# Performance work log

Hardware: AMD Instinct MI355X
Metric: run time of the kernel (lower is better)

The kernel has to match this reference:

```python
import jax, jax.numpy as jnp
import numpy as np

PARAM = 10.0
EPS = 1e-06

def _feature_map(t):
    # elus_feature_map: param*relu(x) + (exp(param*min(x,0)) - 1) + 1
    x1 = jax.nn.relu(t)
    x2 = t - x1  # negative part
    return PARAM * x1 + jnp.exp(PARAM * x2)

def setup_inputs() -> dict:
    key = jax.random.key(0)
    ks = jax.random.split(key, 7)
    B, C, H, W = 8, 512, 128, 128
    d = C // 8
    s = 1.0 / np.sqrt(C)
    return {
        "x":  jax.random.normal(ks[0], (B, C, H, W), dtype=jnp.float32),
        "Wq": jax.random.normal(ks[1], (d, C), dtype=jnp.float32) * s,
        "bq": jax.random.normal(ks[2], (d,), dtype=jnp.float32) * 0.01,
        "Wk": jax.random.normal(ks[3], (d, C), dtype=jnp.float32) * s,
        "bk": jax.random.normal(ks[4], (d,), dtype=jnp.float32) * 0.01,
        "Wv": jax.random.normal(ks[5], (C, C), dtype=jnp.float32) * s,
        "bv": jax.random.normal(ks[6], (C,), dtype=jnp.float32) * 0.01,
        "gamma": jnp.full((1,), 0.5, dtype=jnp.float32),
    }

def reference(x, Wq, bq, Wk, bk, Wv, bv, gamma):
    B, C, H, W = x.shape
    N = H * W
    xf = x.reshape(B, C, N)  # flatten spatial; 1x1 convs become matmuls
    Q = jnp.einsum('dc,bcn->bdn', Wq, xf) + bq[None, :, None]   # [B, d, N]
    K = jnp.einsum('dc,bcn->bdn', Wk, xf) + bk[None, :, None]   # [B, d, N]
    V = jnp.einsum('oc,bcn->bon', Wv, xf) + bv[None, :, None]   # [B, C, N]
    Q = jnp.transpose(_feature_map(Q), (0, 2, 1))               # [B, N, d]
    K = _feature_map(K)                                         # [B, d, N]
    KV = jnp.einsum('bmn,bcn->bmc', K, V)                       # [B, d, C]
    norm = 1.0 / jnp.einsum('bnc,bc->bn', Q, jnp.sum(K, axis=-1) + EPS)  # [B, N]
    wv = jnp.einsum('bnm,bmc,bn->bcn', Q, KV, norm)             # [B, C, N]
    wv = wv.reshape(B, C, H, W)
    return x + gamma * wv
```

## Files before the change

kernel.cpp:

```cpp
#include <hip/hip_runtime.h>
#include <hip/hip_bf16.h>
#include <cstdint>

typedef __bf16 bf16x8 __attribute__((ext_vector_type(8)));
typedef float f32x4 __attribute__((ext_vector_type(4)));

#define DEV static __device__ __forceinline__

constexpr int NB = 8;
constexpr int NC = 512;
constexpr int NS = 16384;
constexpr int ND = 64;
constexpr int SK = 32;
constexpr float FPARAM = 10.0f;
constexpr float FEPS = 1e-6f;

DEV unsigned short f2bf(float f) {
  uint32_t u = __builtin_bit_cast(uint32_t, f);
  u += 0x7fffu + ((u >> 16) & 1u);
  return (unsigned short)(u >> 16);
}
DEV float bf2f(unsigned short h) {
  uint32_t u = ((uint32_t)h) << 16;
  return __builtin_bit_cast(float, u);
}
DEV float fmap(float t) {
  float p = fmaxf(t, 0.0f);
  float m = fminf(t, 0.0f);
  return FPARAM * p + __expf(FPARAM * m);
}

DEV void tile_store4(unsigned short* t, int row, int k, ushort4 v) {
  int ch = (k >> 3) ^ (row & 7);
  *(ushort4*)(t + row * 64 + ch * 8 + (k & 7)) = v;
}
DEV void tile_store8(unsigned short* t, int row, int k, uint4 v) {
  int ch = (k >> 3) ^ (row & 7);
  *(uint4*)(t + row * 64 + ch * 8) = v;
}
DEV bf16x8 tile_frag(const unsigned short* t, int row, int k) {
  int ch = (k >> 3) ^ (row & 7);
  uint4 u = *(const uint4*)(t + row * 64 + ch * 8);
  return __builtin_bit_cast(bf16x8, u);
}
DEV f32x4 mfma16(bf16x8 a, bf16x8 b, f32x4 c) {
  return __builtin_amdgcn_mfma_f32_16x16x32_bf16(a, b, c, 0, 0, 0);
}

__global__ __launch_bounds__(256) void kernelA(
    const float* __restrict__ x, const float* __restrict__ Wq,
    const float* __restrict__ bq, const float* __restrict__ Wk,
    const float* __restrict__ bk, unsigned short* __restrict__ Kp,
    unsigned short* __restrict__ Qt) {
  __shared__ unsigned short sW[128 * 64];
  __shared__ unsigned short sX[128 * 64];
  const int t = threadIdx.x;
  const int lane = t & 63, wave = t >> 6;
  const int wm = wave >> 1, wn = wave & 1;
  const int l15 = lane & 15, q = lane >> 4;
  const int n0 = blockIdx.x * 128;
  const int b = blockIdx.y;
  const float* xb = x + (size_t)b * NC * NS;

  f32x4 acc[4][4];
  const f32x4 zero = {0.f, 0.f, 0.f, 0.f};
  for (int i = 0; i < 4; i++)
    for (int j = 0; j < 4; j++) acc[i][j] = zero;

  const int qq = t & 3, grp = t >> 2;
  const int n4 = (grp & 31) * 4, cb = (grp >> 5) * 4;
  const int shfl_base = (t & 63) & ~3;

  for (int c0 = 0; c0 < NC; c0 += 64) {
    __syncthreads();
    {
      int f4 = t & 15;
      for (int it = 0; it < 8; it++) {
        int row = (t >> 4) + it * 16;
        const float* src = (row < 64) ? (Wq + (size_t)row * NC + c0 + f4 * 4)
                                      : (Wk + (size_t)(row - 64) * NC + c0 + f4 * 4);
        float4 v = *(const float4*)src;
        tile_store4(sW, row, f4 * 4,
                    make_ushort4(f2bf(v.x), f2bf(v.y), f2bf(v.z), f2bf(v.w)));
      }
    }
    for (int it = 0; it < 8; it++) {
      int c_l = cb + qq + it * 8;
      float4 v = *(const float4*)(xb + (size_t)(c0 + c_l) * NS + n0 + n4);
      float vv[4] = {v.x, v.y, v.z, v.w};
      float o[4];
      for (int r = 0; r < 4; r++) {
        int j = (qq + r) & 3;
        float send = vv[(qq - r) & 3];
        o[j] = __shfl(send, shfl_base + j);
      }
      tile_store4(sX, n4 + qq, it * 8 + cb,
                  make_ushort4(f2bf(o[0]), f2bf(o[1]), f2bf(o[2]), f2bf(o[3])));
    }
    __syncthreads();
    for (int kk = 0; kk < 64; kk += 32) {
      int kb = kk + q * 8;
      bf16x8 af[4], bg[4];
      for (int i = 0; i < 4; i++) af[i] = tile_frag(sW, wm * 64 + i * 16 + l15, kb);
      for (int j = 0; j < 4; j++) bg[j] = tile_frag(sX, wn * 64 + j * 16 + l15, kb);
      for (int i = 0; i < 4; i++)
        for (int j = 0; j < 4; j++) acc[i][j] = mfma16(af[i], bg[j], acc[i][j]);
    }
  }

  if (wm == 0) {
    for (int i = 0; i < 4; i++) {
      int mb = i * 16 + q * 4;
      float b0 = bq[mb + 0], b1 = bq[mb + 1], b2 = bq[mb + 2], b3 = bq[mb + 3];
      for (int j = 0; j < 4; j++) {
        int n = n0 + wn * 64 + j * 16 + l15;
        f32x4 v = acc[i][j];
        ushort4 o = make_ushort4(f2bf(fmap(v[0] + b0)), f2bf(fmap(v[1] + b1)),
                                 f2bf(fmap(v[2] + b2)), f2bf(fmap(v[3] + b3)));
        *(ushort4*)(Qt + ((size_t)b * NS + n) * ND + mb) = o;
      }
    }
  } else {
    for (int i = 0; i < 4; i++) {
      int mb = i * 16 + q * 4;
      float b0 = bk[mb + 0], b1 = bk[mb + 1], b2 = bk[mb + 2], b3 = bk[mb + 3];
      for (int j = 0; j < 4; j++) {
        int n = n0 + wn * 64 + j * 16 + l15;
        f32x4 v = acc[i][j];
        Kp[((size_t)b * ND + mb + 0) * NS + n] = f2bf(fmap(v[0] + b0));
        Kp[((size_t)b * ND + mb + 1) * NS + n] = f2bf(fmap(v[1] + b1));
        Kp[((size_t)b * ND + mb + 2) * NS + n] = f2bf(fmap(v[2] + b2));
        Kp[((size_t)b * ND + mb + 3) * NS + n] = f2bf(fmap(v[3] + b3));
      }
    }
  }
}

__global__ __launch_bounds__(256) void kernelB(
    const float* __restrict__ x, const unsigned short* __restrict__ Kp,
    float* __restrict__ Pp, float* __restrict__ KsP) {
  __shared__ unsigned short sK[64 * 64];
  __shared__ unsigned short sX[256 * 64];
  __shared__ float sSum[64];
  const int t = threadIdx.x;
  const int lane = t & 63, wave = t >> 6;
  const int l15 = lane & 15, q = lane >> 4;
  const int s = blockIdx.x, half = blockIdx.y, b = blockIdx.z;
  const int cp0 = half * 256;
  const int nbase = s * (NS / SK);
  if (t < 64) sSum[t] = 0.0f;

  f32x4 acc[4][4];
  const f32x4 zero = {0.f, 0.f, 0.f, 0.f};
  for (int i = 0; i < 4; i++)
    for (int j = 0; j < 4; j++) acc[i][j] = zero;

  for (int nc = 0; nc < NS / SK; nc += 64) {
    int n0 = nbase + nc;
    __syncthreads();
    for (int it = 0; it < 2; it++) {
      int row = (t >> 3) + it * 32;
      int ch = t & 7;
      uint4 v = *(const uint4*)(Kp + ((size_t)b * ND + row) * NS + n0 + ch * 8);
      tile_store8(sK, row, ch * 8, v);
      if (half == 0) {
        const unsigned short* pv = (const unsigned short*)&v;
        float ssum = 0.f;
        for (int e = 0; e < 8; e++) ssum += bf2f(pv[e]);
        atomicAdd(&sSum[row], ssum);
      }
    }
    {
      int f4 = t & 15;
      for (int it = 0; it < 16; it++) {
        int row = (t >> 4) + it * 16;
        float4 v = *(const float4*)(x + ((size_t)b * NC + cp0 + row) * NS + n0 + f4 * 4);
        tile_store4(sX, row, f4 * 4,
                    make_ushort4(f2bf(v.x), f2bf(v.y), f2bf(v.z), f2bf(v.w)));
      }
    }
    __syncthreads();
    for (int kk = 0; kk < 64; kk += 32) {
      int kb = kk + q * 8;
      bf16x8 af[4], bg[4];
      for (int i = 0; i < 4; i++) af[i] = tile_frag(sK, i * 16 + l15, kb);
      for (int j = 0; j < 4; j++) bg[j] = tile_frag(sX, wave * 64 + j * 16 + l15, kb);
      for (int i = 0; i < 4; i++)
        for (int j = 0; j < 4; j++) acc[i][j] = mfma16(af[i], bg[j], acc[i][j]);
    }
  }
  for (int i = 0; i < 4; i++) {
    int mb = i * 16 + q * 4;
    for (int j = 0; j < 4; j++) {
      int cp = cp0 + wave * 64 + j * 16 + l15;
      f32x4 v = acc[i][j];
      for (int r = 0; r < 4; r++)
        Pp[(((size_t)b * SK + s) * ND + mb + r) * NC + cp] = v[r];
    }
  }
  __syncthreads();
  if (half == 0 && t < 64) KsP[((size_t)b * SK + s) * ND + t] = sSum[t];
}

__global__ __launch_bounds__(256) void kernelC1(
    const float* __restrict__ Pp, const float* __restrict__ KsP,
    float* __restrict__ KXt, float* __restrict__ Ksum) {
  const int m = blockIdx.x, b = blockIdx.y, t = threadIdx.x;
  float a0 = 0.f, a1 = 0.f;
  for (int s = 0; s < SK; s++) {
    const float* p = Pp + (((size_t)b * SK + s) * ND + m) * NC;
    a0 += p[t];
    a1 += p[t + 256];
  }
  float* o = KXt + ((size_t)b * ND + m) * NC;
  o[t] = a0;
  o[t + 256] = a1;
  if (t == 0) {
    float ks = 0.f;
    for (int s = 0; s < SK; s++) ks += KsP[((size_t)b * SK + s) * ND + m];
    Ksum[b * ND + m] = ks;
  }
}

__global__ __launch_bounds__(64) void kernelC2(
    const float* __restrict__ KXt, const float* __restrict__ Wv,
    const float* __restrict__ bv, const float* __restrict__ Ksum,
    unsigned short* __restrict__ KVT) {
  __shared__ unsigned short sA[64 * 64];
  __shared__ unsigned short sB[64 * 64];
  const int t = threadIdx.x;
  const int l15 = t & 15, q = t >> 4;
  const int ct = blockIdx.x, b = blockIdx.y;
  f32x4 acc[4][4];
  const f32x4 zero = {0.f, 0.f, 0.f, 0.f};
  for (int i = 0; i < 4; i++)
    for (int j = 0; j < 4; j++) acc[i][j] = zero;

  for (int c0 = 0; c0 < NC; c0 += 64) {
    __syncthreads();
    int f4 = t & 15;
    for (int it = 0; it < 16; it++) {
      int row = (t >> 4) + it * 4;
      float4 v = *(const float4*)(Wv + ((size_t)(ct * 64 + row)) * NC + c0 + f4 * 4);
      tile_store4(sA, row, f4 * 4,
                  make_ushort4(f2bf(v.x), f2bf(v.y), f2bf(v.z), f2bf(v.w)));
      float4 w = *(const float4*)(KXt + ((size_t)b * ND + row) * NC + c0 + f4 * 4);
      tile_store4(sB, row, f4 * 4,
                  make_ushort4(f2bf(w.x), f2bf(w.y), f2bf(w.z), f2bf(w.w)));
    }
    __syncthreads();
    for (int kk = 0; kk < 64; kk += 32) {
      int kb = kk + q * 8;
      bf16x8 af[4], bg[4];
      for (int i = 0; i < 4; i++) af[i] = tile_frag(sA, i * 16 + l15, kb);
      for (int j = 0; j < 4; j++) bg[j] = tile_frag(sB, j * 16 + l15, kb);
      for (int i = 0; i < 4; i++)
        for (int j = 0; j < 4; j++) acc[i][j] = mfma16(af[i], bg[j], acc[i][j]);
    }
  }
  for (int j = 0; j < 4; j++) {
    int m = j * 16 + l15;
    float ks = Ksum[b * ND + m];
    for (int i = 0; i < 4; i++) {
      for (int r = 0; r < 4; r++) {
        int c = ct * 64 + i * 16 + q * 4 + r;
        float v = acc[i][j][r] + ks * bv[c];
        KVT[((size_t)b * NC + c) * ND + m] = f2bf(v);
      }
    }
  }
}

__global__ __launch_bounds__(256) void kernelD(
    const float* __restrict__ x, const unsigned short* __restrict__ Qt,
    const unsigned short* __restrict__ KVT, const float* __restrict__ Ksum,
    const float* __restrict__ gamma, float* __restrict__ out) {
  __shared__ unsigned short sA[256 * 64];
  __shared__ unsigned short sB[128 * 64];
  __shared__ float sN[128];
  __shared__ float sKs[64];
  const int t = threadIdx.x;
  const int lane = t & 63, wave = t >> 6;
  const int wm = wave >> 1, wn = wave & 1;
  const int l15 = lane & 15, q = lane >> 4;
  const int n0 = blockIdx.x * 128;
  const int c0 = blockIdx.y * 256;
  const int b = blockIdx.z;
  if (t < 64) sKs[t] = Ksum[b * ND + t] + FEPS;
  {
    int ch = t & 7;
    for (int it = 0; it < 8; it++) {
      int row = (t >> 3) + it * 32;
      uint4 v = *(const uint4*)(KVT + ((size_t)b * NC + c0 + row) * ND + ch * 8);
      tile_store8(sA, row, ch * 8, v);
    }
    for (int it = 0; it < 4; it++) {
      int row = (t >> 3) + it * 32;
      uint4 v = *(const uint4*)(Qt + ((size_t)b * NS + n0 + row) * ND + ch * 8);
      tile_store8(sB, row, ch * 8, v);
    }
  }
  __syncthreads();
  if (t < 128) {
    float sum = 0.f;
    for (int ch = 0; ch < 8; ch++) {
      const unsigned short* p = sB + t * 64 + ((ch ^ (t & 7)) * 8);
      for (int e = 0; e < 8; e++) sum += bf2f(p[e]) * sKs[ch * 8 + e];
    }
    sN[t] = 1.0f / sum;
  }
  __syncthreads();

  f32x4 acc[8][4];
  const f32x4 zero = {0.f, 0.f, 0.f, 0.f};
  for (int i = 0; i < 8; i++)
    for (int j = 0; j < 4; j++) acc[i][j] = zero;
  for (int kk = 0; kk < 64; kk += 32) {
    int kb = kk + q * 8;
    bf16x8 af[8], bg[4];
    for (int i = 0; i < 8; i++) af[i] = tile_frag(sA, wm * 128 + i * 16 + l15, kb);
    for (int j = 0; j < 4; j++) bg[j] = tile_frag(sB, wn * 64 + j * 16 + l15, kb);
    for (int i = 0; i < 8; i++)
      for (int j = 0; j < 4; j++) acc[i][j] = mfma16(af[i], bg[j], acc[i][j]);
  }
  float g = gamma[0];
  for (int i = 0; i < 8; i++) {
    int cb = c0 + wm * 128 + i * 16 + q * 4;
    for (int j = 0; j < 4; j++) {
      int nl = wn * 64 + j * 16 + l15;
      int n = n0 + nl;
      float nr = sN[nl] * g;
      f32x4 v = acc[i][j];
      for (int r = 0; r < 4; r++) {
        size_t idx = ((size_t)b * NC + cb + r) * NS + n;
        out[idx] = x[idx] + nr * v[r];
      }
    }
  }
}

extern "C" void kernel_launch(void* const* d_in, const int* in_sizes, int n_in,
                              void* d_out, int out_size, void* d_ws, size_t ws_size,
                              hipStream_t stream) {
  (void)in_sizes; (void)n_in; (void)out_size; (void)ws_size;
  const float* x = (const float*)d_in[0];
  const float* Wq = (const float*)d_in[1];
  const float* bq = (const float*)d_in[2];
  const float* Wk = (const float*)d_in[3];
  const float* bk = (const float*)d_in[4];
  const float* Wv = (const float*)d_in[5];
  const float* bv = (const float*)d_in[6];
  const float* gamma = (const float*)d_in[7];
  float* out = (float*)d_out;

  char* ws = (char*)d_ws;
  unsigned short* Qt = (unsigned short*)ws;  ws += (size_t)NB * NS * ND * 2;
  unsigned short* Kp = (unsigned short*)ws;  ws += (size_t)NB * ND * NS * 2;
  float* Pp = (float*)ws;                    ws += (size_t)NB * SK * ND * NC * 4;
  float* KsP = (float*)ws;                   ws += (size_t)NB * SK * ND * 4;
  float* KXt = (float*)ws;                   ws += (size_t)NB * ND * NC * 4;
  float* Ksum = (float*)ws;                  ws += (size_t)NB * ND * 4;
  unsigned short* KVT = (unsigned short*)ws; ws += (size_t)NB * NC * ND * 2;

  kernelA<<<dim3(NS / 128, NB), dim3(256), 0, stream>>>(x, Wq, bq, Wk, bk, Kp, Qt);
  kernelB<<<dim3(SK, 2, NB), dim3(256), 0, stream>>>(x, Kp, Pp, KsP);
  kernelC1<<<dim3(ND, NB), dim3(256), 0, stream>>>(Pp, KsP, KXt, Ksum);
  kernelC2<<<dim3(NC / 64, NB), dim3(64), 0, stream>>>(KXt, Wv, bv, Ksum, KVT);
  kernelD<<<dim3(NS / 128, NC / 256, NB), dim3(256), 0, stream>>>(x, Qt, KVT, Ksum, gamma, out);
}
```

Measured before the change: 640.6 us.

## Fuse Q/K projection with K·X reduction into one kernel per spatial chunk

Merges the old projection kernel and the K·X partial-sum kernel. Each block now handles a 512-wide spatial chunk: it loads x once into shared memory in both layouts, computes Q and K, applies the feature map, keeps K in shared memory, and immediately accumulates K·X^T plus the K sums. This drops the Kp round trip through global memory and the second full read of x. The weights are pre-converted to bf16 by a small new kernel and read straight from global memory. In exchange the kernel uses large shared memory (about 80KB) with 512-thread blocks and only 256 blocks, which may reduce occupancy and parallelism.

```diff
diff --git a/kernel.cpp b/kernel.cpp
--- a/kernel.cpp
+++ b/kernel.cpp
@@ -1,5 +1,4 @@
 #include <hip/hip_runtime.h>
-#include <hip/hip_bf16.h>
 #include <cstdint>
 
 typedef __bf16 bf16x8 __attribute__((ext_vector_type(8)));
@@ -29,6 +28,13 @@
   float m = fminf(t, 0.0f);
   return FPARAM * p + __expf(FPARAM * m);
 }
+DEV f32x4 mfma16(bf16x8 a, bf16x8 b, f32x4 c) {
+  return __builtin_amdgcn_mfma_f32_16x16x32_bf16(a, b, c, 0, 0, 0);
+}
+DEV bf16x8 ld_bf8(const unsigned short* p) {
+  uint4 u = *(const uint4*)p;
+  return __builtin_bit_cast(bf16x8, u);
+}
 
 DEV void tile_store4(unsigned short* t, int row, int k, ushort4 v) {
   int ch = (k >> 3) ^ (row & 7);
@@ -37,169 +43,197 @@
 DEV void tile_store8(unsigned short* t, int row, int k, uint4 v) {
   int ch = (k >> 3) ^ (row & 7);
   *(uint4*)(t + row * 64 + ch * 8) = v;
+}
+DEV void tile_store1(unsigned short* t, int row, int k, unsigned short v) {
+  int ch = (k >> 3) ^ (row & 7);
+  t[row * 64 + ch * 8 + (k & 7)] = v;
 }
 DEV bf16x8 tile_frag(const unsigned short* t, int row, int k) {
   int ch = (k >> 3) ^ (row & 7);
   uint4 u = *(const uint4*)(t + row * 64 + ch * 8);
   return __builtin_bit_cast(bf16x8, u);
 }
-DEV f32x4 mfma16(bf16x8 a, bf16x8 b, f32x4 c) {
-  return __builtin_amdgcn_mfma_f32_16x16x32_bf16(a, b, c, 0, 0, 0);
-}
-
-__global__ __launch_bounds__(256) void kernelA(
-    const float* __restrict__ x, const float* __restrict__ Wq,
-    const float* __restrict__ bq, const float* __restrict__ Wk,
-    const float* __restrict__ bk, unsigned short* __restrict__ Kp,
-    unsigned short* __restrict__ Qt) {
-  __shared__ unsigned short sW[128 * 64];
-  __shared__ unsigned short sX[128 * 64];
-  const int t = threadIdx.x;
-  const int lane = t & 63, wave = t >> 6;
-  const int wm = wave >> 1, wn = wave & 1;
-  const int l15 = lane & 15, q = lane >> 4;
-  const int n0 = blockIdx.x * 128;
-  const int b = blockIdx.y;
-  const float* xb = x + (size_t)b * NC * NS;
-
-  f32x4 acc[4][4];
-  const f32x4 zero = {0.f, 0.f, 0.f, 0.f};
-  for (int i = 0; i < 4; i++)
-    for (int j = 0; j < 4; j++) acc[i][j] = zero;
-
-  const int qq = t & 3, grp = t >> 2;
-  const int n4 = (grp & 31) * 4, cb = (grp >> 5) * 4;
-  const int shfl_base = (t & 63) & ~3;
-
-  for (int c0 = 0; c0 < NC; c0 += 64) {
-    __syncthreads();
-    {
-      int f4 = t & 15;
-      for (int it = 0; it < 8; it++) {
-        int row = (t >> 4) + it * 16;
-        const float* src = (row < 64) ? (Wq + (size_t)row * NC + c0 + f4 * 4)
-                                      : (Wk + (size_t)(row - 64) * NC + c0 + f4 * 4);
-        float4 v = *(const float4*)src;
-        tile_store4(sW, row, f4 * 4,
-                    make_ushort4(f2bf(v.x), f2bf(v.y), f2bf(v.z), f2bf(v.w)));
-      }
-    }
-    for (int it = 0; it < 8; it++) {
-      int c_l = cb + qq + it * 8;
-      float4 v = *(const float4*)(xb + (size_t)(c0 + c_l) * NS + n0 + n4);
-      float vv[4] = {v.x, v.y, v.z, v.w};
-      float o[4];
-      for (int r = 0; r < 4; r++) {
-        int j = (qq + r) & 3;
-        float send = vv[(qq - r) & 3];
-        o[j] = __shfl(send, shfl_base + j);
-      }
-      tile_store4(sX, n4 + qq, it * 8 + cb,
-                  make_ushort4(f2bf(o[0]), f2bf(o[1]), f2bf(o[2]), f2bf(o[3])));
-    }
-    __syncthreads();
-    for (int kk = 0; kk < 64; kk += 32) {
-      int kb = kk + q * 8;
-      bf16x8 af[4], bg[4];
-      for (int i = 0; i < 4; i++) af[i] = tile_frag(sW, wm * 64 + i * 16 + l15, kb);
-      for (int j = 0; j < 4; j++) bg[j] = tile_frag(sX, wn * 64 + j * 16 + l15, kb);
-      for (int i = 0; i < 4; i++)
-        for (int j = 0; j < 4; j++) acc[i][j] = mfma16(af[i], bg[j], acc[i][j]);
-    }
-  }
-
-  if (wm == 0) {
-    for (int i = 0; i < 4; i++) {
-      int mb = i * 16 + q * 4;
-      float b0 = bq[mb + 0], b1 = bq[mb + 1], b2 = bq[mb + 2], b3 = bq[mb + 3];
-      for (int j = 0; j < 4; j++) {
-        int n = n0 + wn * 64 + j * 16 + l15;
-        f32x4 v = acc[i][j];
-        ushort4 o = make_ushort4(f2bf(fmap(v[0] + b0)), f2bf(fmap(v[1] + b1)),
-                                 f2bf(fmap(v[2] + b2)), f2bf(fmap(v[3] + b3)));
-        *(ushort4*)(Qt + ((size_t)b * NS + n) * ND + mb) = o;
-      }
-    }
-  } else {
-    for (int i = 0; i < 4; i++) {
-      int mb = i * 16 + q * 4;
-      float b0 = bk[mb + 0], b1 = bk[mb + 1], b2 = bk[mb + 2], b3 = bk[mb + 3];
-      for (int j = 0; j < 4; j++) {
-        int n = n0 + wn * 64 + j * 16 + l15;
-        f32x4 v = acc[i][j];
-        Kp[((size_t)b * ND + mb + 0) * NS + n] = f2bf(fmap(v[0] + b0));
-        Kp[((size_t)b * ND + mb + 1) * NS + n] = f2bf(fmap(v[1] + b1));
-        Kp[((size_t)b * ND + mb + 2) * NS + n] = f2bf(fmap(v[2] + b2));
-        Kp[((size_t)b * ND + mb + 3) * NS + n] = f2bf(fmap(v[3] + b3));
-      }
-    }
-  }
-}
-
-__global__ __launch_bounds__(256) void kernelB(
-    const float* __restrict__ x, const unsigned short* __restrict__ Kp,
-    float* __restrict__ Pp, float* __restrict__ KsP) {
-  __shared__ unsigned short sK[64 * 64];
-  __shared__ unsigned short sX[256 * 64];
-  __shared__ float sSum[64];
+DEV uint4 tile_frag_u(const unsigned short* t, int row, int k) {
+  int ch = (k >> 3) ^ (row & 7);
+  return *(const uint4*)(t + row * 64 + ch * 8);
+}
+
+__global__ __launch_bounds__(256) void kernelP(
+    const float* __restrict__ Wq, const float* __restrict__ Wk,
+    unsigned short* __restrict__ Wqkb) {
+  const int tid = blockIdx.x * 256 + threadIdx.x;
+  const int stride = gridDim.x * 256;
+  for (int p = tid; p < ND * NC / 4; p += stride) {
+    float4 v = ((const float4*)Wq)[p];
+    ((ushort4*)Wqkb)[p] = make_ushort4(f2bf(v.x), f2bf(v.y), f2bf(v.z), f2bf(v.w));
+  }
+  for (int p = tid; p < ND * NC / 4; p += stride) {
+    float4 v = ((const float4*)Wk)[p];
+    ((ushort4*)(Wqkb + ND * NC))[p] =
+        make_ushort4(f2bf(v.x), f2bf(v.y), f2bf(v.z), f2bf(v.w));
+  }
+}
+
+__global__ __launch_bounds__(512) void kernelA(
+    const float* __restrict__ x, const unsigned short* __restrict__ Wqk,
+    const float* __restrict__ bq, const float* __restrict__ bk,
+    unsigned short* __restrict__ Qt, float* __restrict__ Pp,
+    float* __restrict__ KsP) {
+  __shared__ unsigned short sXN[512 * 64];
+  __shared__ unsigned short sXT[2][64 * 64];
+  __shared__ float sKs[64];
+  unsigned short* sKp = sXT[0];
+  unsigned short* sQt = sXT[1];
+
   const int t = threadIdx.x;
   const int lane = t & 63, wave = t >> 6;
   const int l15 = lane & 15, q = lane >> 4;
-  const int s = blockIdx.x, half = blockIdx.y, b = blockIdx.z;
-  const int cp0 = half * 256;
-  const int nbase = s * (NS / SK);
-  if (t < 64) sSum[t] = 0.0f;
-
-  f32x4 acc[4][4];
+  const int wm = wave >> 1, wn = wave & 1;
+  const int w2m = wave >> 2, w2c = wave & 3;
+  const int s = blockIdx.x, b = blockIdx.y;
+  const int nbase = s * 512;
+  const float* xb = x + (size_t)b * NC * NS;
+
+  float bias[2][4];
+  {
+    const float* bb = (wm < 2) ? bq : bk;
+    int mb = (wm & 1) * 32;
+    for (int i = 0; i < 2; i++)
+      for (int r = 0; r < 4; r++) bias[i][r] = bb[mb + i * 16 + q * 4 + r];
+  }
+  if (t < 64) sKs[t] = 0.f;
+
+  const int qq = t & 3, grp = t >> 2;
+  const int n4 = (grp & 15) * 4;
+  const int cb4 = (grp >> 4) * 4;
+  const int shfl_base = lane & ~3;
+
+  f32x4 acc2[2][8];
   const f32x4 zero = {0.f, 0.f, 0.f, 0.f};
-  for (int i = 0; i < 4; i++)
-    for (int j = 0; j < 4; j++) acc[i][j] = zero;
-
-  for (int nc = 0; nc < NS / SK; nc += 64) {
-    int n0 = nbase + nc;
+  for (int i = 0; i < 2; i++)
+    for (int j = 0; j < 8; j++) acc2[i][j] = zero;
+
+  for (int nch = 0; nch < 8; nch++) {
+    const int n0l = nch * 64;
+    f32x4 acc1[2][2];
+    for (int i = 0; i < 2; i++)
+      for (int j = 0; j < 2; j++) acc1[i][j] = zero;
+
+    for (int cs = 0; cs < 8; cs++) {
+      const int c0 = cs * 64;
+      unsigned short* xt = sXT[cs & 1];
+#pragma unroll
+      for (int it = 0; it < 2; it++) {
+        int c_l = cb4 + qq + it * 32;
+        float4 v = *(const float4*)(xb + (size_t)(c0 + c_l) * NS + nbase + n0l + n4);
+        tile_store4(sXN, c0 + c_l, n4,
+                    make_ushort4(f2bf(v.x), f2bf(v.y), f2bf(v.z), f2bf(v.w)));
+        float vv[4] = {v.x, v.y, v.z, v.w};
+        float o[4];
+#pragma unroll
+        for (int r = 0; r < 4; r++) {
+          int j = (qq + r) & 3;
+          float send = vv[(qq - r) & 3];
+          o[j] = __shfl(send, shfl_base + j);
+        }
+        tile_store4(xt, n4 + qq, cb4 + it * 32,
+                    make_ushort4(f2bf(o[0]), f2bf(o[1]), f2bf(o[2]), f2bf(o[3])));
+      }
+      __syncthreads();
+#pragma unroll
+      for (int kk = 0; kk < 64; kk += 32) {
+        int kb = kk + q * 8;
+        bf16x8 af[2], bg[2];
+#pragma unroll
+        for (int i = 0; i < 2; i++)
+          af[i] = ld_bf8(Wqk + (size_t)(wm * 32 + i * 16 + l15) * NC + c0 + kb);
+#pragma unroll
+        for (int j = 0; j < 2; j++)
+          bg[j] = tile_frag(xt, wn * 32 + j * 16 + l15, kb);
+#pragma unroll
+        for (int i = 0; i < 2; i++)
+#pragma unroll
+          for (int j = 0; j < 2; j++) acc1[i][j] = mfma16(af[i], bg[j], acc1[i][j]);
+      }
+    }
     __syncthreads();
-    for (int it = 0; it < 2; it++) {
-      int row = (t >> 3) + it * 32;
-      int ch = t & 7;
-      uint4 v = *(const uint4*)(Kp + ((size_t)b * ND + row) * NS + n0 + ch * 8);
-      tile_store8(sK, row, ch * 8, v);
-      if (half == 0) {
-        const unsigned short* pv = (const unsigned short*)&v;
-        float ssum = 0.f;
-        for (int e = 0; e < 8; e++) ssum += bf2f(pv[e]);
-        atomicAdd(&sSum[row], ssum);
+
+    if (wm >= 2) {
+      int mrow = (wm - 2) * 32;
+#pragma unroll
+      for (int i = 0; i < 2; i++) {
+        float ks[4] = {0.f, 0.f, 0.f, 0.f};
+#pragma unroll
+        for (int j = 0; j < 2; j++) {
+          int nl = wn * 32 + j * 16 + l15;
+#pragma unroll
+          for (int r = 0; r < 4; r++) {
+            float f = fmap(acc1[i][j][r] + bias[i][r]);
+            tile_store1(sKp, mrow + i * 16 + q * 4 + r, nl, f2bf(f));
+            ks[r] += f;
+          }
+        }
+#pragma unroll
+        for (int ms = 1; ms < 16; ms <<= 1)
+#pragma unroll
+          for (int r = 0; r < 4; r++) ks[r] += __shfl_xor(ks[r], ms);
+        if (l15 == 0)
+#pragma unroll
+          for (int r = 0; r < 4; r++)
+            atomicAdd(&sKs[mrow + i * 16 + q * 4 + r], ks[r]);
       }
-    }
+    } else {
+      int mrow = wm * 32;
+#pragma unroll
+      for (int i = 0; i < 2; i++)
+#pragma unroll
+        for (int j = 0; j < 2; j++) {
+          int nl = wn * 32 + j * 16 + l15;
+          ushort4 o;
+          o.x = f2bf(fmap(acc1[i][j][0] + bias[i][0]));
+          o.y = f2bf(fmap(acc1[i][j][1] + bias[i][1]));
+          o.z = f2bf(fmap(acc1[i][j][2] + bias[i][2]));
+          o.w = f2bf(fmap(acc1[i][j][3] + bias[i][3]));
+          tile_store4(sQt, nl, mrow + i * 16 + q * 4, o);
+        }
+    }
+    __syncthreads();
     {
-      int f4 = t & 15;
-      for (int it = 0; it < 16; it++) {
-        int row = (t >> 4) + it * 16;
-        float4 v = *(const float4*)(x + ((size_t)b * NC + cp0 + row) * NS + n0 + f4 * 4);
-        tile_store4(sX, row, f4 * 4,
-                    make_ushort4(f2bf(v.x), f2bf(v.y), f2bf(v.z), f2bf(v.w)));
-      }
-    }
-    __syncthreads();
+      int nr = t >> 3, m0 = (t & 7) * 8;
+      uint4 u = tile_frag_u(sQt, nr, m0);
+      *(uint4*)(Qt + ((size_t)b * NS + nbase + n0l + nr) * ND + m0) = u;
+    }
+#pragma unroll
     for (int kk = 0; kk < 64; kk += 32) {
       int kb = kk + q * 8;
-      bf16x8 af[4], bg[4];
-      for (int i = 0; i < 4; i++) af[i] = tile_frag(sK, i * 16 + l15, kb);
-      for (int j = 0; j < 4; j++) bg[j] = tile_frag(sX, wave * 64 + j * 16 + l15, kb);
-      for (int i = 0; i < 4; i++)
-        for (int j = 0; j < 4; j++) acc[i][j] = mfma16(af[i], bg[j], acc[i][j]);
-    }
-  }
-  for (int i = 0; i < 4; i++) {
-    int mb = i * 16 + q * 4;
-    for (int j = 0; j < 4; j++) {
-      int cp = cp0 + wave * 64 + j * 16 + l15;
-      f32x4 v = acc[i][j];
-      for (int r = 0; r < 4; r++)
-        Pp[(((size_t)b * SK + s) * ND + mb + r) * NC + cp] = v[r];
-    }
-  }
-  __syncthreads();
-  if (half == 0 && t < 64) KsP[((size_t)b * SK + s) * ND + t] = sSum[t];
+      bf16x8 af[2], bg[8];
+#pragma unroll
+      for (int i = 0; i < 2; i++)
+        af[i] = tile_frag(sKp, w2m * 32 + i * 16 + l15, kb);
+#pragma unroll
+      for (int j = 0; j < 8; j++)
+        bg[j] = tile_frag(sXN, w2c * 128 + j * 16 + l15, kb);
+#pragma unroll
+      for (int i = 0; i < 2; i++)
+#pragma unroll
+        for (int j = 0; j < 8; j++) acc2[i][j] = mfma16(af[i], bg[j], acc2[i][j]);
+    }
+    __syncthreads();
+  }
+
+  float* pp = Pp + ((size_t)b * SK + s) * ND * NC;
+#pragma unroll
+  for (int i = 0; i < 2; i++) {
+    int mb = w2m * 32 + i * 16 + q * 4;
+#pragma unroll
+    for (int j = 0; j < 8; j++) {
+      int cp = w2c * 128 + j * 16 + l15;
+      f32x4 v = acc2[i][j];
+#pragma unroll
+      for (int r = 0; r < 4; r++) pp[(size_t)(mb + r) * NC + cp] = v[r];
+    }
+  }
+  if (t < 64) KsP[((size_t)b * SK + s) * ND + t] = sKs[t];
 }
 
 __global__ __launch_bounds__(256) void kernelC1(
@@ -207,6 +241,7 @@
     float* __restrict__ KXt, float* __restrict__ Ksum) {
   const int m = blockIdx.x, b = blockIdx.y, t = threadIdx.x;
   float a0 = 0.f, a1 = 0.f;
+#pragma unroll 8
   for (int s = 0; s < SK; s++) {
     const float* p = Pp + (((size_t)b * SK + s) * ND + m) * NC;
     a0 += p[t];
@@ -354,16 +389,16 @@
   float* out = (float*)d_out;
 
   char* ws = (char*)d_ws;
-  unsigned short* Qt = (unsigned short*)ws;  ws += (size_t)NB * NS * ND * 2;
-  unsigned short* Kp = (unsigned short*)ws;  ws += (size_t)NB * ND * NS * 2;
-  float* Pp = (float*)ws;                    ws += (size_t)NB * SK * ND * NC * 4;
-  float* KsP = (float*)ws;                   ws += (size_t)NB * SK * ND * 4;
-  float* KXt = (float*)ws;                   ws += (size_t)NB * ND * NC * 4;
-  float* Ksum = (float*)ws;                  ws += (size_t)NB * ND * 4;
-  unsigned short* KVT = (unsigned short*)ws; ws += (size_t)NB * NC * ND * 2;
-
-  kernelA<<<dim3(NS / 128, NB), dim3(256), 0, stream>>>(x, Wq, bq, Wk, bk, Kp, Qt);
-  kernelB<<<dim3(SK, 2, NB), dim3(256), 0, stream>>>(x, Kp, Pp, KsP);
+  unsigned short* Qt = (unsigned short*)ws;   ws += (size_t)NB * NS * ND * 2;
+  float* Pp = (float*)ws;                     ws += (size_t)NB * SK * ND * NC * 4;
+  float* KsP = (float*)ws;                    ws += (size_t)NB * SK * ND * 4;
+  float* KXt = (float*)ws;                    ws += (size_t)NB * ND * NC * 4;
+  float* Ksum = (float*)ws;                   ws += (size_t)NB * ND * 4;
+  unsigned short* KVT = (unsigned short*)ws;  ws += (size_t)NB * NC * ND * 2;
+  unsigned short* Wqkb = (unsigned short*)ws; ws += (size_t)2 * ND * NC * 2;
+
+  kernelP<<<dim3(32), dim3(256), 0, stream>>>(Wq, Wk, Wqkb);
+  kernelA<<<dim3(SK, NB), dim3(512), 0, stream>>>(x, Wqkb, bq, bk, Qt, Pp, KsP);
   kernelC1<<<dim3(ND, NB), dim3(256), 0, stream>>>(Pp, KsP, KXt, Ksum);
   kernelC2<<<dim3(NC / 64, NB), dim3(64), 0, stream>>>(KXt, Wv, bv, Ksum, KVT);
   kernelD<<<dim3(NS / 128, NC / 256, NB), dim3(256), 0, stream>>>(x, Qt, KVT, Ksum, gamma, out);
```

Result: slower. 674.6 us (+5.3%).
